# Kernel optimization log

Measured on AMD Instinct MI355X. Metric: run time of the kernel, lower is better.

Reference implementation:

```python
import jax, jax.numpy as jnp
import numpy as np

N_USER, N_ITEM, D = 50000, 30000, 64
N = N_USER + N_ITEM
NNZ_UI, NNZ_R, NNZ_II = 1000000, 800000, 300000
IMG_F, TXT_F = 512, 384
EPS = 1e-5


def spmm(rows, cols, vals, x, n_out):
    # sparse [n_out, n_in] @ dense [n_in, d] via gather + segment-sum
    return jax.ops.segment_sum(vals[:, None] * x[cols], rows, num_segments=n_out)


def leaky_relu(x):
    return jnp.where(x >= 0, x, 0.01 * x)


def setup_inputs() -> dict:
    key = jax.random.key(0)
    ks = jax.random.split(key, 32)
    f = lambda i, shape, s=0.05: (jax.random.normal(ks[i], shape, dtype=jnp.float32) * s)
    inp = {
        'user_emb': f(0, (N_USER, D)),
        'item_emb': f(1, (N_ITEM, D)),
        'image_embedding': f(2, (N_ITEM, IMG_F), 1.0),
        'text_embedding': f(3, (N_ITEM, TXT_F), 1.0),
        'W_img': f(4, (IMG_F, D)), 'b_img': jnp.zeros((D,), jnp.float32),
        'bn_g_img': jnp.ones((D,), jnp.float32), 'bn_b_img': jnp.zeros((D,), jnp.float32),
        'W_txt': f(5, (TXT_F, D)), 'b_txt': jnp.zeros((D,), jnp.float32),
        'bn_g_txt': jnp.ones((D,), jnp.float32), 'bn_b_txt': jnp.zeros((D,), jnp.float32),
        'W_gate_img': f(6, (D, D)), 'b_gate_img': jnp.zeros((D,), jnp.float32),
        'W_gate_txt': f(7, (D, D)), 'b_gate_txt': jnp.zeros((D,), jnp.float32),
        'W_common1': f(8, (D, D)), 'b_common1': jnp.zeros((D,), jnp.float32),
        'w_common2': f(9, (D,)),
        'ui_vals': jax.random.uniform(ks[10], (NNZ_UI,), dtype=jnp.float32),
        'R_vals': jax.random.uniform(ks[11], (NNZ_R,), dtype=jnp.float32),
        'ii_img_vals': jax.random.uniform(ks[12], (NNZ_II,), dtype=jnp.float32),
        'ii_txt_vals': jax.random.uniform(ks[13], (NNZ_II,), dtype=jnp.float32),
        'ui_rows': jax.random.randint(ks[14], (NNZ_UI,), 0, N, dtype=jnp.int32),
        'ui_cols': jax.random.randint(ks[15], (NNZ_UI,), 0, N, dtype=jnp.int32),
        'R_rows': jax.random.randint(ks[16], (NNZ_R,), 0, N_USER, dtype=jnp.int32),
        'R_cols': jax.random.randint(ks[17], (NNZ_R,), 0, N_ITEM, dtype=jnp.int32),
        'ii_img_rows': jax.random.randint(ks[18], (NNZ_II,), 0, N_ITEM, dtype=jnp.int32),
        'ii_img_cols': jax.random.randint(ks[19], (NNZ_II,), 0, N_ITEM, dtype=jnp.int32),
        'ii_txt_rows': jax.random.randint(ks[20], (NNZ_II,), 0, N_ITEM, dtype=jnp.int32),
        'ii_txt_cols': jax.random.randint(ks[21], (NNZ_II,), 0, N_ITEM, dtype=jnp.int32),
    }
    return inp


def reference(user_emb, item_emb, image_embedding, text_embedding,
              W_img, b_img, bn_g_img, bn_b_img,
              W_txt, b_txt, bn_g_txt, bn_b_txt,
              W_gate_img, b_gate_img, W_gate_txt, b_gate_txt,
              W_common1, b_common1, w_common2,
              ui_vals, R_vals, ii_img_vals, ii_txt_vals,
              ui_rows, ui_cols, R_rows, R_cols,
              ii_img_rows, ii_img_cols, ii_txt_rows, ii_txt_cols):
    # ---- user_item_GCN: adj = original + diffusion (fused edge list) ----
    cat = jnp.concatenate([item_emb, user_emb], axis=0)  # [N, D], item first per source
    embs = [cat]
    for _ in range(2):
        cat = spmm(ui_rows, ui_cols, ui_vals, cat, N)
        embs.append(cat)
    content_embedding = jnp.stack(embs, axis=1).mean(axis=1)  # [N, D]

    # ---- modal projections (BN inference, dropout=eval identity) ----
    def project(x, W, b, g, beta):
        h = x @ W + b
        h = h * (g / jnp.sqrt(1.0 + EPS)) + beta  # BatchNorm1d, running stats (0, 1)
        return leaky_relu(h)

    img_feat = project(image_embedding, W_img, b_img, bn_g_img, bn_b_img)  # [I, D]
    txt_feat = project(text_embedding, W_txt, b_txt, bn_g_txt, bn_b_txt)

    # ---- item_item_GCN ----
    def modal_branch(feat, Wg, bg, rows, cols, vals):
        it = item_emb * jax.nn.sigmoid(feat @ Wg + bg)  # gated item embedding
        for _ in range(2):
            it = spmm(rows, cols, vals, it, N_ITEM)
        us = spmm(R_rows, R_cols, R_vals, it, N_USER)  # R @ item -> user
        return jnp.concatenate([us, it], axis=0)  # [N, D], user first per source

    image_ui = modal_branch(img_feat, W_gate_img, b_gate_img, ii_img_rows, ii_img_cols, ii_img_vals)
    text_ui = modal_branch(txt_feat, W_gate_txt, b_gate_txt, ii_txt_rows, ii_txt_cols, ii_txt_vals)

    # ---- gate_attention_fusion (non-tiktok: 2 modalities) ----
    def att_score(e):
        return leaky_relu(e @ W_common1 + b_common1) @ w_common2  # [N]

    att = jnp.stack([att_score(image_ui), att_score(text_ui)], axis=-1)  # [N, 2]
    w = jax.nn.softmax(att, axis=-1)
    common = w[:, 0:1] * image_ui + w[:, 1:2] * text_ui
    special_img = image_ui - common
    special_txt = text_ui - common

    return jnp.stack([content_embedding, special_img, special_txt, common], axis=0)  # [4, N, D]
```

## Files before the change

kernel.cpp:

```cpp
#include <hip/hip_runtime.h>

#define N_USER 50000
#define N_ITEM 30000
#define DIM    64
#define NTOT   80000
#define NNZ_UI 1000000
#define NNZ_R  800000
#define NNZ_II 300000
#define IMG_F  512
#define TXT_F  384

#define NROWS_ALL 190000
#define NNZ_ALL   2400000
#define BASE_R    NTOT
#define BASE_II   (NTOT + N_USER)
#define BASE_IT   (NTOT + N_USER + N_ITEM)

#define RB_BITS   9
#define RB_ROWS   512
#define NBUCK     ((NROWS_ALL + RB_ROWS - 1) / RB_ROWS)
#define NBLK_A2   400
#define EDG_A2    6000

#define NBLK_PG   625
#define NBLK_UIP  5000
#define NBLK_I16  1875
#define NBLK_U16  3125

__device__ __forceinline__ int edge_row(int i,
        const int* __restrict__ r0, const int* __restrict__ r1,
        const int* __restrict__ r2, const int* __restrict__ r3){
    if (i < NNZ_UI)                       return r0[i];
    if (i < NNZ_UI + NNZ_R)               return BASE_R  + r1[i - NNZ_UI];
    if (i < NNZ_UI + NNZ_R + NNZ_II)      return BASE_II + r2[i - NNZ_UI - NNZ_R];
    return BASE_IT + r3[i - NNZ_UI - NNZ_R - NNZ_II];
}

__device__ __forceinline__ void edge_all(int i,
        const int* __restrict__ r0, const int* __restrict__ c0, const float* __restrict__ v0,
        const int* __restrict__ r1, const int* __restrict__ c1, const float* __restrict__ v1,
        const int* __restrict__ r2, const int* __restrict__ c2, const float* __restrict__ v2,
        const int* __restrict__ r3, const int* __restrict__ c3, const float* __restrict__ v3,
        int& gr, int& col, float& val){
    if (i < NNZ_UI){
        gr = r0[i]; col = c0[i]; val = v0[i];
    } else if (i < NNZ_UI + NNZ_R){
        int j = i - NNZ_UI;               gr = BASE_R  + r1[j]; col = c1[j]; val = v1[j];
    } else if (i < NNZ_UI + NNZ_R + NNZ_II){
        int j = i - NNZ_UI - NNZ_R;       gr = BASE_II + r2[j]; col = c2[j]; val = v2[j];
    } else {
        int j = i - NNZ_UI - NNZ_R - NNZ_II; gr = BASE_IT + r3[j]; col = c3[j]; val = v3[j];
    }
}

__global__ __launch_bounds__(256) void k_bhist(const int* __restrict__ r0,
        const int* __restrict__ r1, const int* __restrict__ r2,
        const int* __restrict__ r3, int* __restrict__ bcnt){
    __shared__ int h[NBUCK];
    for (int i = threadIdx.x; i < NBUCK; i += 256) h[i] = 0;
    __syncthreads();
    const int stride = gridDim.x * 256;
    for (int i = blockIdx.x * 256 + threadIdx.x; i < NNZ_ALL; i += stride){
        int gr = edge_row(i, r0, r1, r2, r3);
        atomicAdd(&h[gr >> RB_BITS], 1);
    }
    __syncthreads();
    for (int i = threadIdx.x; i < NBUCK; i += 256){
        int c = h[i];
        if (c) atomicAdd(&bcnt[i], c);
    }
}

__global__ __launch_bounds__(512) void k_bscan(const int* __restrict__ bcnt,
        int* __restrict__ bbase, int* __restrict__ off){
    __shared__ int sh[512];
    const int t = threadIdx.x;
    int v = (t < NBUCK) ? bcnt[t] : 0;
    sh[t] = v;
    __syncthreads();
    for (int d = 1; d < 512; d <<= 1){
        int u = (t >= d) ? sh[t - d] : 0;
        __syncthreads();
        sh[t] += u;
        __syncthreads();
    }
    if (t < NBUCK) bbase[t] = sh[t] - v;
    if (t == NBUCK - 1){
        bbase[NBUCK] = sh[t];
        off[NROWS_ALL] = sh[t];
    }
}

__global__ __launch_bounds__(256) void k_bin(
        const int* __restrict__ r0, const int* __restrict__ c0, const float* __restrict__ v0,
        const int* __restrict__ r1, const int* __restrict__ c1, const float* __restrict__ v1,
        const int* __restrict__ r2, const int* __restrict__ c2, const float* __restrict__ v2,
        const int* __restrict__ r3, const int* __restrict__ c3, const float* __restrict__ v3,
        const int* __restrict__ bbase, int* __restrict__ bcur,
        int2* __restrict__ binned){
    __shared__ int lofs[NBUCK];
    __shared__ int lcur[NBUCK];
    const int t = threadIdx.x;
    for (int i = t; i < NBUCK; i += 256){ lofs[i] = 0; lcur[i] = 0; }
    __syncthreads();
    const int s0 = blockIdx.x * EDG_A2, s1 = s0 + EDG_A2;
    for (int i = s0 + t; i < s1; i += 256){
        int gr = edge_row(i, r0, r1, r2, r3);
        atomicAdd(&lofs[gr >> RB_BITS], 1);
    }
    __syncthreads();
    for (int i = t; i < NBUCK; i += 256){
        int c = lofs[i];
        lofs[i] = c ? (bbase[i] + atomicAdd(&bcur[i], c)) : 0;
    }
    __syncthreads();
    for (int i = s0 + t; i < s1; i += 256){
        int gr, col; float val;
        edge_all(i, r0, c0, v0, r1, c1, v1, r2, c2, v2, r3, c3, v3, gr, col, val);
        int b = gr >> RB_BITS;
        int slot = atomicAdd(&lcur[b], 1);
        binned[lofs[b] + slot] = make_int2((col << RB_BITS) | (gr & (RB_ROWS - 1)),
                                           __float_as_int(val));
    }
}

__global__ __launch_bounds__(256) void k_scatter(const int* __restrict__ bbase,
        const int2* __restrict__ binned, int* __restrict__ off,
        int2* __restrict__ csr){
    __shared__ int h[RB_ROWS];
    const int t = threadIdx.x;
    const int b = blockIdx.x;
    const int base = bbase[b];
    const int nb = bbase[b + 1] - base;
    h[t] = 0; h[t + 256] = 0;
    __syncthreads();
    for (int i = t; i < nb; i += 256)
        atomicAdd(&h[binned[base + i].x & (RB_ROWS - 1)], 1);
    __syncthreads();
    if (t < 64){
        int v[8], s = 0;
#pragma unroll
        for (int k = 0; k < 8; ++k){ v[k] = h[t * 8 + k]; s += v[k]; }
        int incl = s;
#pragma unroll
        for (int d = 1; d < 64; d <<= 1){
            int u = __shfl_up(incl, d, 64);
            if (t >= d) incl += u;
        }
        int run = incl - s;
#pragma unroll
        for (int k = 0; k < 8; ++k){ int tmp = v[k]; h[t * 8 + k] = run; run += tmp; }
    }
    __syncthreads();
    const int row0 = b << RB_BITS;
    for (int i = t; i < RB_ROWS; i += 256){
        int r = row0 + i;
        if (r < NROWS_ALL) off[r] = base + h[i];
    }
    __syncthreads();
    for (int i = t; i < nb; i += 256){
        int2 rec = binned[base + i];
        int lr = rec.x & (RB_ROWS - 1);
        int slot = atomicAdd(&h[lr], 1);
        csr[base + slot] = make_int2(rec.x >> RB_BITS, rec.y);
    }
}

__device__ __forceinline__ const float* cat_row(int c,
        const float* __restrict__ item, const float* __restrict__ user){
    return (c < N_ITEM) ? (item + ((long)c << 6)) : (user + ((long)(c - N_ITEM) << 6));
}

__device__ __forceinline__ void pull_body(const int* __restrict__ off,
        const int2* __restrict__ csr, const float* __restrict__ x,
        float* __restrict__ y, int r, int l){
    int s = off[r], e = off[r + 1];
    float4 a0 = {0.f, 0.f, 0.f, 0.f};
    float4 a1 = {0.f, 0.f, 0.f, 0.f};
    int j = s;
    for (; j + 2 <= e; j += 2){
        int2 e0 = csr[j];
        int2 e1 = csr[j + 1];
        float v0 = __int_as_float(e0.y);
        float v1 = __int_as_float(e1.y);
        const float4 x0 = *reinterpret_cast<const float4*>(x + ((long)e0.x << 6) + l);
        const float4 x1 = *reinterpret_cast<const float4*>(x + ((long)e1.x << 6) + l);
        a0.x = fmaf(v0, x0.x, a0.x);
        a0.y = fmaf(v0, x0.y, a0.y);
        a0.z = fmaf(v0, x0.z, a0.z);
        a0.w = fmaf(v0, x0.w, a0.w);
        a1.x = fmaf(v1, x1.x, a1.x);
        a1.y = fmaf(v1, x1.y, a1.y);
        a1.z = fmaf(v1, x1.z, a1.z);
        a1.w = fmaf(v1, x1.w, a1.w);
    }
    if (j < e){
        int2 e0 = csr[j];
        float v0 = __int_as_float(e0.y);
        const float4 x0 = *reinterpret_cast<const float4*>(x + ((long)e0.x << 6) + l);
        a0.x = fmaf(v0, x0.x, a0.x);
        a0.y = fmaf(v0, x0.y, a0.y);
        a0.z = fmaf(v0, x0.z, a0.z);
        a0.w = fmaf(v0, x0.w, a0.w);
    }
    a0.x += a1.x; a0.y += a1.y; a0.z += a1.z; a0.w += a1.w;
    *reinterpret_cast<float4*>(y + ((long)r << 6) + l) = a0;
}

__device__ __forceinline__ void pull_cat_body(const int* __restrict__ off,
        const int2* __restrict__ csr, const float* __restrict__ item,
        const float* __restrict__ user, float* __restrict__ y, int r, int l){
    int s = off[r], e = off[r + 1];
    float4 a0 = {0.f, 0.f, 0.f, 0.f};
    float4 a1 = {0.f, 0.f, 0.f, 0.f};
    int j = s;
    for (; j + 2 <= e; j += 2){
        int2 e0 = csr[j];
        int2 e1 = csr[j + 1];
        float v0 = __int_as_float(e0.y);
        float v1 = __int_as_float(e1.y);
        const float4 x0 = *reinterpret_cast<const float4*>(cat_row(e0.x, item, user) + l);
        const float4 x1 = *reinterpret_cast<const float4*>(cat_row(e1.x, item, user) + l);
        a0.x = fmaf(v0, x0.x, a0.x);
        a0.y = fmaf(v0, x0.y, a0.y);
        a0.z = fmaf(v0, x0.z, a0.z);
        a0.w = fmaf(v0, x0.w, a0.w);
        a1.x = fmaf(v1, x1.x, a1.x);
        a1.y = fmaf(v1, x1.y, a1.y);
        a1.z = fmaf(v1, x1.z, a1.z);
        a1.w = fmaf(v1, x1.w, a1.w);
    }
    if (j < e){
        int2 e0 = csr[j];
        float v0 = __int_as_float(e0.y);
        const float4 x0 = *reinterpret_cast<const float4*>(cat_row(e0.x, item, user) + l);
        a0.x = fmaf(v0, x0.x, a0.x);
        a0.y = fmaf(v0, x0.y, a0.y);
        a0.z = fmaf(v0, x0.z, a0.z);
        a0.w = fmaf(v0, x0.w, a0.w);
    }
    a0.x += a1.x; a0.y += a1.y; a0.z += a1.z; a0.w += a1.w;
    *reinterpret_cast<float4*>(y + ((long)r << 6) + l) = a0;
}

__global__ void k_pull2(const int* __restrict__ offA, const int2* __restrict__ csr,
                        const float* __restrict__ xA, float* __restrict__ yA,
                        const int* __restrict__ offB, const float* __restrict__ xB,
                        float* __restrict__ yB, int nrows, int nblk_half){
    int b = blockIdx.x;
    const int* off; const float* x; float* y;
    if (b < nblk_half){ off = offA; x = xA; y = yA; }
    else              { b -= nblk_half; off = offB; x = xB; y = yB; }
    int t = b * 256 + threadIdx.x;
    int r = t >> 4;
    if (r >= nrows) return;
    pull_body(off, csr, x, y, r, (t & 15) << 2);
}

__global__ void k_pullR(const int* __restrict__ off, const int2* __restrict__ csr,
                        const float* __restrict__ xA, float* __restrict__ yA,
                        const float* __restrict__ xB, float* __restrict__ yB,
                        int nrows){
    int t = blockIdx.x * 256 + threadIdx.x;
    int r = t >> 4;
    if (r >= nrows) return;
    int l = (t & 15) << 2;
    int s = off[r], e = off[r + 1];
    float4 pA0 = {0.f,0.f,0.f,0.f}, pA1 = {0.f,0.f,0.f,0.f};
    float4 pB0 = {0.f,0.f,0.f,0.f}, pB1 = {0.f,0.f,0.f,0.f};
    int j = s;
    for (; j + 2 <= e; j += 2){
        int2 e0 = csr[j];
        int2 e1 = csr[j + 1];
        float v0 = __int_as_float(e0.y);
        float v1 = __int_as_float(e1.y);
        long o0 = ((long)e0.x << 6) + l;
        long o1 = ((long)e1.x << 6) + l;
        const float4 xa0 = *reinterpret_cast<const float4*>(xA + o0);
        const float4 xa1 = *reinterpret_cast<const float4*>(xA + o1);
        const float4 xb0 = *reinterpret_cast<const float4*>(xB + o0);
        const float4 xb1 = *reinterpret_cast<const float4*>(xB + o1);
        pA0.x = fmaf(v0, xa0.x, pA0.x); pA0.y = fmaf(v0, xa0.y, pA0.y);
        pA0.z = fmaf(v0, xa0.z, pA0.z); pA0.w = fmaf(v0, xa0.w, pA0.w);
        pA1.x = fmaf(v1, xa1.x, pA1.x); pA1.y = fmaf(v1, xa1.y, pA1.y);
        pA1.z = fmaf(v1, xa1.z, pA1.z); pA1.w = fmaf(v1, xa1.w, pA1.w);
        pB0.x = fmaf(v0, xb0.x, pB0.x); pB0.y = fmaf(v0, xb0.y, pB0.y);
        pB0.z = fmaf(v0, xb0.z, pB0.z); pB0.w = fmaf(v0, xb0.w, pB0.w);
        pB1.x = fmaf(v1, xb1.x, pB1.x); pB1.y = fmaf(v1, xb1.y, pB1.y);
        pB1.z = fmaf(v1, xb1.z, pB1.z); pB1.w = fmaf(v1, xb1.w, pB1.w);
    }
    if (j < e){
        int2 e0 = csr[j];
        float v0 = __int_as_float(e0.y);
        long o0 = ((long)e0.x << 6) + l;
        const float4 xa0 = *reinterpret_cast<const float4*>(xA + o0);
        const float4 xb0 = *reinterpret_cast<const float4*>(xB + o0);
        pA0.x = fmaf(v0, xa0.x, pA0.x); pA0.y = fmaf(v0, xa0.y, pA0.y);
        pA0.z = fmaf(v0, xa0.z, pA0.z); pA0.w = fmaf(v0, xa0.w, pA0.w);
        pB0.x = fmaf(v0, xb0.x, pB0.x); pB0.y = fmaf(v0, xb0.y, pB0.y);
        pB0.z = fmaf(v0, xb0.z, pB0.z); pB0.w = fmaf(v0, xb0.w, pB0.w);
    }
    pA0.x += pA1.x; pA0.y += pA1.y; pA0.z += pA1.z; pA0.w += pA1.w;
    pB0.x += pB1.x; pB0.y += pB1.y; pB0.z += pB1.z; pB0.w += pB1.w;
    *reinterpret_cast<float4*>(yA + ((long)r << 6) + l) = pA0;
    *reinterpret_cast<float4*>(yB + ((long)r << 6) + l) = pB0;
}

__global__ void k_pull_mean_cat(const int* __restrict__ off, const int2* __restrict__ csr,
        const float* __restrict__ x, const float* __restrict__ item,
        const float* __restrict__ user, float* __restrict__ o0, int nrows){
    int t = blockIdx.x * 256 + threadIdx.x;
    int r = t >> 4;
    if (r >= nrows) return;
    int l = (t & 15) << 2;
    int s = off[r], e = off[r + 1];
    float4 a0 = {0.f, 0.f, 0.f, 0.f};
    float4 a1 = {0.f, 0.f, 0.f, 0.f};
    int j = s;
    for (; j + 2 <= e; j += 2){
        int2 e0 = csr[j];
        int2 e1 = csr[j + 1];
        float v0 = __int_as_float(e0.y);
        float v1 = __int_as_float(e1.y);
        const float4 x0 = *reinterpret_cast<const float4*>(x + ((long)e0.x << 6) + l);
        const float4 x1 = *reinterpret_cast<const float4*>(x + ((long)e1.x << 6) + l);
        a0.x = fmaf(v0, x0.x, a0.x);
        a0.y = fmaf(v0, x0.y, a0.y);
        a0.z = fmaf(v0, x0.z, a0.z);
        a0.w = fmaf(v0, x0.w, a0.w);
        a1.x = fmaf(v1, x1.x, a1.x);
        a1.y = fmaf(v1, x1.y, a1.y);
        a1.z = fmaf(v1, x1.z, a1.z);
        a1.w = fmaf(v1, x1.w, a1.w);
    }
    if (j < e){
        int2 e0 = csr[j];
        float v0 = __int_as_float(e0.y);
        const float4 x0 = *reinterpret_cast<const float4*>(x + ((long)e0.x << 6) + l);
        a0.x = fmaf(v0, x0.x, a0.x);
        a0.y = fmaf(v0, x0.y, a0.y);
        a0.z = fmaf(v0, x0.z, a0.z);
        a0.w = fmaf(v0, x0.w, a0.w);
    }
    const float4 av = *reinterpret_cast<const float4*>(cat_row(r, item, user) + l);
    const float4 xv = *reinterpret_cast<const float4*>(x + ((long)r << 6) + l);
    float4 o;
    o.x = (av.x + xv.x + a0.x + a1.x) * (1.0f / 3.0f);
    o.y = (av.y + xv.y + a0.y + a1.y) * (1.0f / 3.0f);
    o.z = (av.z + xv.z + a0.z + a1.z) * (1.0f / 3.0f);
    o.w = (av.w + xv.w + a0.w + a1.w) * (1.0f / 3.0f);
    *reinterpret_cast<float4*>(o0 + ((long)r << 6) + l) = o;
}

__global__ __launch_bounds__(256) void k_mega1(
        const int* __restrict__ offUI, const int2* __restrict__ csr,
        const float* __restrict__ user,
        float* __restrict__ hop1out,
        const float* __restrict__ Xi, const float* __restrict__ Wi,
        const float* __restrict__ bi, const float* __restrict__ gi,
        const float* __restrict__ bei, const float* __restrict__ Wgi,
        const float* __restrict__ bgi,
        const float* __restrict__ Xt, const float* __restrict__ Wt,
        const float* __restrict__ bt, const float* __restrict__ gt,
        const float* __restrict__ bet, const float* __restrict__ Wgt,
        const float* __restrict__ bgt,
        const float* __restrict__ item,
        float* __restrict__ Pi, float* __restrict__ Pt){
    __shared__ float xs[48][68];
    __shared__ float ws[64][64];

    if (blockIdx.x < NBLK_UIP){
        int t = blockIdx.x * 256 + threadIdx.x;
        int r = t >> 4;
        pull_cat_body(offUI, csr, item, user, hop1out, r, (t & 15) << 2);
        return;
    }

    const int t  = threadIdx.x;
    const int tr = t >> 4;
    const int tc = t & 15;
    const int pgb = blockIdx.x - NBLK_UIP;
    const bool isTxt = pgb >= NBLK_PG;
    const int  blk   = isTxt ? (pgb - NBLK_PG) : pgb;
    const int  K     = isTxt ? TXT_F : IMG_F;
    const float* X   = isTxt ? Xt  : Xi;
    const float* W   = isTxt ? Wt  : Wi;
    const float* bb  = isTxt ? bt  : bi;
    const float* gg  = isTxt ? gt  : gi;
    const float* be  = isTxt ? bet : bei;
    const float* Wg  = isTxt ? Wgt : Wgi;
    const float* bg  = isTxt ? bgt : bgi;
    float* outP      = isTxt ? Pt  : Pi;
    const int row0   = blk * 48;

    float acc[3][4];
#pragma unroll
    for (int i = 0; i < 3; ++i)
#pragma unroll
        for (int j = 0; j < 4; ++j) acc[i][j] = 0.f;

    for (int ks = 0; ks < K; ks += 64){
        __syncthreads();
#pragma unroll
        for (int i = 0; i < 3; ++i){
            int r = tr + 16 * i;
            *reinterpret_cast<float4*>(&xs[r][tc * 4]) =
                *reinterpret_cast<const float4*>(X + (long)(row0 + r) * K + ks + tc * 4);
        }
        {
            const float4* wsrc = reinterpret_cast<const float4*>(W + (long)ks * 64);
            float4* wdst = reinterpret_cast<float4*>(&ws[0][0]);
#pragma unroll
            for (int i = 0; i < 4; ++i) wdst[t + 256 * i] = wsrc[t + 256 * i];
        }
        __syncthreads();
#pragma unroll 8
        for (int kk = 0; kk < 64; kk += 2){
            float2 a[3];
#pragma unroll
            for (int i = 0; i < 3; ++i)
                a[i] = *reinterpret_cast<const float2*>(&xs[tr + 16 * i][kk]);
            float4 b0 = *reinterpret_cast<const float4*>(&ws[kk][tc * 4]);
            float4 b1 = *reinterpret_cast<const float4*>(&ws[kk + 1][tc * 4]);
#pragma unroll
            for (int i = 0; i < 3; ++i){
                acc[i][0] = fmaf(a[i].x, b0.x, acc[i][0]);
                acc[i][1] = fmaf(a[i].x, b0.y, acc[i][1]);
                acc[i][2] = fmaf(a[i].x, b0.z, acc[i][2]);
                acc[i][3] = fmaf(a[i].x, b0.w, acc[i][3]);
                acc[i][0] = fmaf(a[i].y, b1.x, acc[i][0]);
                acc[i][1] = fmaf(a[i].y, b1.y, acc[i][1]);
                acc[i][2] = fmaf(a[i].y, b1.z, acc[i][2]);
                acc[i][3] = fmaf(a[i].y, b1.w, acc[i][3]);
            }
        }
    }

    const float4 b4  = reinterpret_cast<const float4*>(bb)[tc];
    const float4 g4  = reinterpret_cast<const float4*>(gg)[tc];
    const float4 be4 = reinterpret_cast<const float4*>(be)[tc];
    __syncthreads();
#pragma unroll
    for (int i = 0; i < 3; ++i){
        int r = tr + 16 * i;
        float4 h;
        h.x = (acc[i][0] + b4.x) * (g4.x * 0.99999500003749943f) + be4.x;
        h.y = (acc[i][1] + b4.y) * (g4.y * 0.99999500003749943f) + be4.y;
        h.z = (acc[i][2] + b4.z) * (g4.z * 0.99999500003749943f) + be4.z;
        h.w = (acc[i][3] + b4.w) * (g4.w * 0.99999500003749943f) + be4.w;
        h.x = (h.x >= 0.f) ? h.x : 0.01f * h.x;
        h.y = (h.y >= 0.f) ? h.y : 0.01f * h.y;
        h.z = (h.z >= 0.f) ? h.z : 0.01f * h.z;
        h.w = (h.w >= 0.f) ? h.w : 0.01f * h.w;
        *reinterpret_cast<float4*>(&xs[r][tc * 4]) = h;
    }
    {
        const float4* wsrc = reinterpret_cast<const float4*>(Wg);
        float4* wdst = reinterpret_cast<float4*>(&ws[0][0]);
#pragma unroll
        for (int i = 0; i < 4; ++i) wdst[t + 256 * i] = wsrc[t + 256 * i];
    }
    __syncthreads();

    float ac2[3][4];
#pragma unroll
    for (int i = 0; i < 3; ++i)
#pragma unroll
        for (int j = 0; j < 4; ++j) ac2[i][j] = 0.f;
#pragma unroll 8
    for (int kk = 0; kk < 64; kk += 2){
        float2 a[3];
#pragma unroll
        for (int i = 0; i < 3; ++i)
            a[i] = *reinterpret_cast<const float2*>(&xs[tr + 16 * i][kk]);
        float4 b0 = *reinterpret_cast<const float4*>(&ws[kk][tc * 4]);
        float4 b1 = *reinterpret_cast<const float4*>(&ws[kk + 1][tc * 4]);
#pragma unroll
        for (int i = 0; i < 3; ++i){
            ac2[i][0] = fmaf(a[i].x, b0.x, ac2[i][0]);
            ac2[i][1] = fmaf(a[i].x, b0.y, ac2[i][1]);
            ac2[i][2] = fmaf(a[i].x, b0.z, ac2[i][2]);
            ac2[i][3] = fmaf(a[i].x, b0.w, ac2[i][3]);
            ac2[i][0] = fmaf(a[i].y, b1.x, ac2[i][0]);
            ac2[i][1] = fmaf(a[i].y, b1.y, ac2[i][1]);
            ac2[i][2] = fmaf(a[i].y, b1.z, ac2[i][2]);
            ac2[i][3] = fmaf(a[i].y, b1.w, ac2[i][3]);
        }
    }

    const float4 bg4 = reinterpret_cast<const float4*>(bg)[tc];
#pragma unroll
    for (int i = 0; i < 3; ++i){
        int r = tr + 16 * i;
        const float4 iv = *reinterpret_cast<const float4*>(
                item + (long)(row0 + r) * 64 + tc * 4);
        float4 o;
        o.x = iv.x / (1.f + __expf(-(ac2[i][0] + bg4.x)));
        o.y = iv.y / (1.f + __expf(-(ac2[i][1] + bg4.y)));
        o.z = iv.z / (1.f + __expf(-(ac2[i][2] + bg4.z)));
        o.w = iv.w / (1.f + __expf(-(ac2[i][3] + bg4.w)));
        *reinterpret_cast<float4*>(outP + (long)(row0 + r) * 64 + tc * 4) = o;
    }
}

__global__ __launch_bounds__(256) void k_fuse(const float* __restrict__ img,
        const float* __restrict__ txt, const float* __restrict__ W1,
        const float* __restrict__ b1, const float* __restrict__ w2,
        float* __restrict__ out){
    __shared__ float si[64][68];
    __shared__ float st[64][68];
    __shared__ float w1s[64][64];
    const int t  = threadIdx.x;
    const int tr = t >> 4;
    const int tc = t & 15;
    const long row0 = (long)blockIdx.x * 64;

#pragma unroll
    for (int i = 0; i < 4; ++i){
        int r = tr + 16 * i;
        *reinterpret_cast<float4*>(&si[r][tc * 4]) =
            *reinterpret_cast<const float4*>(img + (row0 + r) * 64 + tc * 4);
        *reinterpret_cast<float4*>(&st[r][tc * 4]) =
            *reinterpret_cast<const float4*>(txt + (row0 + r) * 64 + tc * 4);
    }
    {
        const float4* wsrc = reinterpret_cast<const float4*>(W1);
        float4* wdst = reinterpret_cast<float4*>(&w1s[0][0]);
#pragma unroll
        for (int i = 0; i < 4; ++i) wdst[t + 256 * i] = wsrc[t + 256 * i];
    }
    __syncthreads();

    float ai[4][4], at[4][4];
#pragma unroll
    for (int i = 0; i < 4; ++i)
#pragma unroll
        for (int j = 0; j < 4; ++j){ ai[i][j] = 0.f; at[i][j] = 0.f; }

#pragma unroll 8
    for (int kk = 0; kk < 64; kk += 2){
        float4 b0 = *reinterpret_cast<const float4*>(&w1s[kk][tc * 4]);
        float4 b1v = *reinterpret_cast<const float4*>(&w1s[kk + 1][tc * 4]);
#pragma unroll
        for (int i = 0; i < 4; ++i){
            float2 a = *reinterpret_cast<const float2*>(&si[tr + 16 * i][kk]);
            float2 c = *reinterpret_cast<const float2*>(&st[tr + 16 * i][kk]);
            ai[i][0] = fmaf(a.x, b0.x, ai[i][0]);
            ai[i][1] = fmaf(a.x, b0.y, ai[i][1]);
            ai[i][2] = fmaf(a.x, b0.z, ai[i][2]);
            ai[i][3] = fmaf(a.x, b0.w, ai[i][3]);
            ai[i][0] = fmaf(a.y, b1v.x, ai[i][0]);
            ai[i][1] = fmaf(a.y, b1v.y, ai[i][1]);
            ai[i][2] = fmaf(a.y, b1v.z, ai[i][2]);
            ai[i][3] = fmaf(a.y, b1v.w, ai[i][3]);
            at[i][0] = fmaf(c.x, b0.x, at[i][0]);
            at[i][1] = fmaf(c.x, b0.y, at[i][1]);
            at[i][2] = fmaf(c.x, b0.z, at[i][2]);
            at[i][3] = fmaf(c.x, b0.w, at[i][3]);
            at[i][0] = fmaf(c.y, b1v.x, at[i][0]);
            at[i][1] = fmaf(c.y, b1v.y, at[i][1]);
            at[i][2] = fmaf(c.y, b1v.z, at[i][2]);
            at[i][3] = fmaf(c.y, b1v.w, at[i][3]);
        }
    }

    const float4 b14 = reinterpret_cast<const float4*>(b1)[tc];
    const float4 w24 = reinterpret_cast<const float4*>(w2)[tc];
    float pi[4], pt[4];
#pragma unroll
    for (int i = 0; i < 4; ++i){
        float hi0 = ai[i][0] + b14.x; hi0 = (hi0 >= 0.f) ? hi0 : 0.01f * hi0;
        float hi1 = ai[i][1] + b14.y; hi1 = (hi1 >= 0.f) ? hi1 : 0.01f * hi1;
        float hi2 = ai[i][2] + b14.z; hi2 = (hi2 >= 0.f) ? hi2 : 0.01f * hi2;
        float hi3 = ai[i][3] + b14.w; hi3 = (hi3 >= 0.f) ? hi3 : 0.01f * hi3;
        float ht0 = at[i][0] + b14.x; ht0 = (ht0 >= 0.f) ? ht0 : 0.01f * ht0;
        float ht1 = at[i][1] + b14.y; ht1 = (ht1 >= 0.f) ? ht1 : 0.01f * ht1;
        float ht2 = at[i][2] + b14.z; ht2 = (ht2 >= 0.f) ? ht2 : 0.01f * ht2;
        float ht3 = at[i][3] + b14.w; ht3 = (ht3 >= 0.f) ? ht3 : 0.01f * ht3;
        pi[i] = fmaf(hi0, w24.x, fmaf(hi1, w24.y, fmaf(hi2, w24.z, hi3 * w24.w)));
        pt[i] = fmaf(ht0, w24.x, fmaf(ht1, w24.y, fmaf(ht2, w24.z, ht3 * w24.w)));
    }
#pragma unroll
    for (int m = 1; m < 16; m <<= 1){
#pragma unroll
        for (int i = 0; i < 4; ++i){
            pi[i] += __shfl_xor(pi[i], m, 64);
            pt[i] += __shfl_xor(pt[i], m, 64);
        }
    }

    const long NTD = (long)NTOT * DIM;
#pragma unroll
    for (int i = 0; i < 4; ++i){
        int r = tr + 16 * i;
        float mx = fmaxf(pi[i], pt[i]);
        float ei = __expf(pi[i] - mx), et = __expf(pt[i] - mx);
        float inv = 1.f / (ei + et);
        float wi = ei * inv, wt = et * inv;
        const float4 ie = *reinterpret_cast<const float4*>(&si[r][tc * 4]);
        const float4 te = *reinterpret_cast<const float4*>(&st[r][tc * 4]);
        float4 cm, oi, ot;
        cm.x = wi * ie.x + wt * te.x;
        cm.y = wi * ie.y + wt * te.y;
        cm.z = wi * ie.z + wt * te.z;
        cm.w = wi * ie.w + wt * te.w;
        oi.x = ie.x - cm.x; oi.y = ie.y - cm.y; oi.z = ie.z - cm.z; oi.w = ie.w - cm.w;
        ot.x = te.x - cm.x; ot.y = te.y - cm.y; ot.z = te.z - cm.z; ot.w = te.w - cm.w;
        long o = (row0 + r) * 64 + tc * 4;
        *reinterpret_cast<float4*>(out + NTD + o)     = oi;
        *reinterpret_cast<float4*>(out + 2 * NTD + o) = ot;
        *reinterpret_cast<float4*>(out + 3 * NTD + o) = cm;
    }
}

extern "C" void kernel_launch(void* const* d_in, const int* in_sizes, int n_in,
                              void* d_out, int out_size, void* d_ws, size_t ws_size,
                              hipStream_t stream){
    const float* user_emb  = (const float*)d_in[0];
    const float* item_emb  = (const float*)d_in[1];
    const float* image_emb = (const float*)d_in[2];
    const float* text_emb  = (const float*)d_in[3];
    const float* W_img = (const float*)d_in[4];
    const float* b_img = (const float*)d_in[5];
    const float* g_img = (const float*)d_in[6];
    const float* be_img= (const float*)d_in[7];
    const float* W_txt = (const float*)d_in[8];
    const float* b_txt = (const float*)d_in[9];
    const float* g_txt = (const float*)d_in[10];
    const float* be_txt= (const float*)d_in[11];
    const float* W_gi  = (const float*)d_in[12];
    const float* b_gi  = (const float*)d_in[13];
    const float* W_gt  = (const float*)d_in[14];
    const float* b_gt  = (const float*)d_in[15];
    const float* W_c1  = (const float*)d_in[16];
    const float* b_c1  = (const float*)d_in[17];
    const float* w_c2  = (const float*)d_in[18];
    const float* ui_vals = (const float*)d_in[19];
    const float* R_vals  = (const float*)d_in[20];
    const float* ii_iv   = (const float*)d_in[21];
    const float* ii_tv   = (const float*)d_in[22];
    const int* ui_rows = (const int*)d_in[23];
    const int* ui_cols = (const int*)d_in[24];
    const int* R_rows  = (const int*)d_in[25];
    const int* R_cols  = (const int*)d_in[26];
    const int* ii_ir   = (const int*)d_in[27];
    const int* ii_ic   = (const int*)d_in[28];
    const int* ii_tr   = (const int*)d_in[29];
    const int* ii_tc   = (const int*)d_in[30];

    const long ND = (long)NTOT * DIM;
    const long ID = (long)N_ITEM * DIM;
    const long UD = (long)N_USER * DIM;

    float* out = (float*)d_out;
    float* o0 = out;
    float* o1 = out + ND;
    float* o2 = out + 2 * ND;
    float* o3 = out + 3 * ND;

    float* P_img = o3;
    float* P_txt = o3 + ID;
    float* Q_img = o2;
    float* Q_txt = o1;

    int2* binned = (int2*)o0;

    int2* csr   = (int2*)d_ws;
    int*  off   = (int*)(csr + NNZ_ALL);
    int*  bcnt  = off + NROWS_ALL + 4;
    int*  bcur  = bcnt + NBUCK;
    int*  bbase = bcur + NBUCK;

    hipMemsetAsync(bcnt, 0, 2 * NBUCK * sizeof(int), stream);
    k_bhist<<<512, 256, 0, stream>>>(ui_rows, R_rows, ii_ir, ii_tr, bcnt);
    k_bscan<<<1, 512, 0, stream>>>(bcnt, bbase, off);
    k_bin<<<NBLK_A2, 256, 0, stream>>>(
        ui_rows, ui_cols, ui_vals,  R_rows, R_cols, R_vals,
        ii_ir, ii_ic, ii_iv,        ii_tr, ii_tc, ii_tv,
        bbase, bcur, binned);
    k_scatter<<<NBUCK, 256, 0, stream>>>(bbase, binned, off, csr);

    const int* offUI = off;
    const int* offR  = off + BASE_R;
    const int* offI2 = off + BASE_II;
    const int* offT2 = off + BASE_IT;

    k_mega1<<<NBLK_UIP + 2 * NBLK_PG, 256, 0, stream>>>(
        offUI, csr, user_emb, o2,
        image_emb, W_img, b_img, g_img, be_img, W_gi, b_gi,
        text_emb,  W_txt, b_txt, g_txt, be_txt, W_gt, b_gt,
        item_emb, P_img, P_txt);

    k_pull_mean_cat<<<NBLK_UIP, 256, 0, stream>>>(
        offUI, csr, o2, item_emb, user_emb, o0, NTOT);

    k_pull2<<<2 * NBLK_I16, 256, 0, stream>>>(
        offI2, csr, P_img, Q_img, offT2, P_txt, Q_txt, N_ITEM, NBLK_I16);
    k_pull2<<<2 * NBLK_I16, 256, 0, stream>>>(
        offI2, csr, Q_img, o1 + UD, offT2, Q_txt, o2 + UD, N_ITEM, NBLK_I16);
    k_pullR<<<NBLK_U16, 256, 0, stream>>>(
        offR, csr, o1 + UD, o1, o2 + UD, o2, N_USER);

    k_fuse<<<NTOT / 64, 256, 0, stream>>>(o1, o2, W_c1, b_c1, w_c2, out);
}
```

Baseline: 562.9 us.

## Fuse first item-item hop with mean pull and interleave block types

The mean/concat pull over the UI graph now runs in one kernel with the first item-item SpMM hop for both modalities, with blocks interleaved 4:3. Block ordering in the first mega kernel is interleaved 4:1 between pull blocks and projection blocks so the two work types overlap. Intermediate buffers are remapped so the second hop writes to scratch in o3. The final R-pull kernel also copies the item rows into the outputs, which drops one launch but adds an explicit copy of the item embeddings.

```diff
diff --git a/kernel.cpp b/kernel.cpp
--- a/kernel.cpp
+++ b/kernel.cpp
@@ -26,6 +26,11 @@
 #define NBLK_UIP  5000
 #define NBLK_I16  1875
 #define NBLK_U16  3125
+#define NBLK_CP   1875
+
+#define NBLK_M1   (NBLK_UIP + 2 * NBLK_PG)
+#define NBLK_M2   (NBLK_UIP + 2 * NBLK_I16)
+#define NBLK_RC   (NBLK_U16 + 2 * NBLK_CP)
 
 __device__ __forceinline__ int edge_row(int i,
         const int* __restrict__ r0, const int* __restrict__ r1,
@@ -243,6 +248,49 @@
     *reinterpret_cast<float4*>(y + ((long)r << 6) + l) = a0;
 }
 
+__device__ __forceinline__ void pull_mean_body(const int* __restrict__ off,
+        const int2* __restrict__ csr, const float* __restrict__ x,
+        const float* __restrict__ item, const float* __restrict__ user,
+        float* __restrict__ o0, int r, int l){
+    int s = off[r], e = off[r + 1];
+    float4 a0 = {0.f, 0.f, 0.f, 0.f};
+    float4 a1 = {0.f, 0.f, 0.f, 0.f};
+    int j = s;
+    for (; j + 2 <= e; j += 2){
+        int2 e0 = csr[j];
+        int2 e1 = csr[j + 1];
+        float v0 = __int_as_float(e0.y);
+        float v1 = __int_as_float(e1.y);
+        const float4 x0 = *reinterpret_cast<const float4*>(x + ((long)e0.x << 6) + l);
+        const float4 x1 = *reinterpret_cast<const float4*>(x + ((long)e1.x << 6) + l);
+        a0.x = fmaf(v0, x0.x, a0.x);
+        a0.y = fmaf(v0, x0.y, a0.y);
+        a0.z = fmaf(v0, x0.z, a0.z);
+        a0.w = fmaf(v0, x0.w, a0.w);
+        a1.x = fmaf(v1, x1.x, a1.x);
+        a1.y = fmaf(v1, x1.y, a1.y);
+        a1.z = fmaf(v1, x1.z, a1.z);
+        a1.w = fmaf(v1, x1.w, a1.w);
+    }
+    if (j < e){
+        int2 e0 = csr[j];
+        float v0 = __int_as_float(e0.y);
+        const float4 x0 = *reinterpret_cast<const float4*>(x + ((long)e0.x << 6) + l);
+        a0.x = fmaf(v0, x0.x, a0.x);
+        a0.y = fmaf(v0, x0.y, a0.y);
+        a0.z = fmaf(v0, x0.z, a0.z);
+        a0.w = fmaf(v0, x0.w, a0.w);
+    }
+    const float4 av = *reinterpret_cast<const float4*>(cat_row(r, item, user) + l);
+    const float4 xv = *reinterpret_cast<const float4*>(x + ((long)r << 6) + l);
+    float4 o;
+    o.x = (av.x + xv.x + a0.x + a1.x) * (1.0f / 3.0f);
+    o.y = (av.y + xv.y + a0.y + a1.y) * (1.0f / 3.0f);
+    o.z = (av.z + xv.z + a0.z + a1.z) * (1.0f / 3.0f);
+    o.w = (av.w + xv.w + a0.w + a1.w) * (1.0f / 3.0f);
+    *reinterpret_cast<float4*>(o0 + ((long)r << 6) + l) = o;
+}
+
 __global__ void k_pull2(const int* __restrict__ offA, const int2* __restrict__ csr,
                         const float* __restrict__ xA, float* __restrict__ yA,
                         const int* __restrict__ offB, const float* __restrict__ xB,
@@ -257,13 +305,207 @@
     pull_body(off, csr, x, y, r, (t & 15) << 2);
 }
 
-__global__ void k_pullR(const int* __restrict__ off, const int2* __restrict__ csr,
-                        const float* __restrict__ xA, float* __restrict__ yA,
-                        const float* __restrict__ xB, float* __restrict__ yB,
-                        int nrows){
-    int t = blockIdx.x * 256 + threadIdx.x;
+__global__ __launch_bounds__(256) void k_mega1(
+        const int* __restrict__ offUI, const int2* __restrict__ csr,
+        const float* __restrict__ user,
+        float* __restrict__ hop1out,
+        const float* __restrict__ Xi, const float* __restrict__ Wi,
+        const float* __restrict__ bi, const float* __restrict__ gi,
+        const float* __restrict__ bei, const float* __restrict__ Wgi,
+        const float* __restrict__ bgi,
+        const float* __restrict__ Xt, const float* __restrict__ Wt,
+        const float* __restrict__ bt, const float* __restrict__ gt,
+        const float* __restrict__ bet, const float* __restrict__ Wgt,
+        const float* __restrict__ bgt,
+        const float* __restrict__ item,
+        float* __restrict__ Pi, float* __restrict__ Pt){
+    __shared__ float xs[48][68];
+    __shared__ float ws[64][64];
+
+    const int r5 = blockIdx.x % 5;
+    const int q5 = blockIdx.x / 5;
+
+    if (r5 < 4){
+        int pb = q5 * 4 + r5;
+        int t = pb * 256 + threadIdx.x;
+        int r = t >> 4;
+        pull_cat_body(offUI, csr, item, user, hop1out, r, (t & 15) << 2);
+        return;
+    }
+
+    const int t  = threadIdx.x;
+    const int tr = t >> 4;
+    const int tc = t & 15;
+    const int pgb = q5;
+    const bool isTxt = pgb >= NBLK_PG;
+    const int  blk   = isTxt ? (pgb - NBLK_PG) : pgb;
+    const int  K     = isTxt ? TXT_F : IMG_F;
+    const float* X   = isTxt ? Xt  : Xi;
+    const float* W   = isTxt ? Wt  : Wi;
+    const float* bb  = isTxt ? bt  : bi;
+    const float* gg  = isTxt ? gt  : gi;
+    const float* be  = isTxt ? bet : bei;
+    const float* Wg  = isTxt ? Wgt : Wgi;
+    const float* bg  = isTxt ? bgt : bgi;
+    float* outP      = isTxt ? Pt  : Pi;
+    const int row0   = blk * 48;
+
+    float acc[3][4];
+#pragma unroll
+    for (int i = 0; i < 3; ++i)
+#pragma unroll
+        for (int j = 0; j < 4; ++j) acc[i][j] = 0.f;
+
+    for (int ks = 0; ks < K; ks += 64){
+        __syncthreads();
+#pragma unroll
+        for (int i = 0; i < 3; ++i){
+            int r = tr + 16 * i;
+            *reinterpret_cast<float4*>(&xs[r][tc * 4]) =
+                *reinterpret_cast<const float4*>(X + (long)(row0 + r) * K + ks + tc * 4);
+        }
+        {
+            const float4* wsrc = reinterpret_cast<const float4*>(W + (long)ks * 64);
+            float4* wdst = reinterpret_cast<float4*>(&ws[0][0]);
+#pragma unroll
+            for (int i = 0; i < 4; ++i) wdst[t + 256 * i] = wsrc[t + 256 * i];
+        }
+        __syncthreads();
+#pragma unroll 8
+        for (int kk = 0; kk < 64; kk += 2){
+            float2 a[3];
+#pragma unroll
+            for (int i = 0; i < 3; ++i)
+                a[i] = *reinterpret_cast<const float2*>(&xs[tr + 16 * i][kk]);
+            float4 b0 = *reinterpret_cast<const float4*>(&ws[kk][tc * 4]);
+            float4 b1 = *reinterpret_cast<const float4*>(&ws[kk + 1][tc * 4]);
+#pragma unroll
+            for (int i = 0; i < 3; ++i){
+                acc[i][0] = fmaf(a[i].x, b0.x, acc[i][0]);
+                acc[i][1] = fmaf(a[i].x, b0.y, acc[i][1]);
+                acc[i][2] = fmaf(a[i].x, b0.z, acc[i][2]);
+                acc[i][3] = fmaf(a[i].x, b0.w, acc[i][3]);
+                acc[i][0] = fmaf(a[i].y, b1.x, acc[i][0]);
+                acc[i][1] = fmaf(a[i].y, b1.y, acc[i][1]);
+                acc[i][2] = fmaf(a[i].y, b1.z, acc[i][2]);
+                acc[i][3] = fmaf(a[i].y, b1.w, acc[i][3]);
+            }
+        }
+    }
+
+    const float4 b4  = reinterpret_cast<const float4*>(bb)[tc];
+    const float4 g4  = reinterpret_cast<const float4*>(gg)[tc];
+    const float4 be4 = reinterpret_cast<const float4*>(be)[tc];
+    __syncthreads();
+#pragma unroll
+    for (int i = 0; i < 3; ++i){
+        int r = tr + 16 * i;
+        float4 h;
+        h.x = (acc[i][0] + b4.x) * (g4.x * 0.99999500003749943f) + be4.x;
+        h.y = (acc[i][1] + b4.y) * (g4.y * 0.99999500003749943f) + be4.y;
+        h.z = (acc[i][2] + b4.z) * (g4.z * 0.99999500003749943f) + be4.z;
+        h.w = (acc[i][3] + b4.w) * (g4.w * 0.99999500003749943f) + be4.w;
+        h.x = (h.x >= 0.f) ? h.x : 0.01f * h.x;
+        h.y = (h.y >= 0.f) ? h.y : 0.01f * h.y;
+        h.z = (h.z >= 0.f) ? h.z : 0.01f * h.z;
+        h.w = (h.w >= 0.f) ? h.w : 0.01f * h.w;
+        *reinterpret_cast<float4*>(&xs[r][tc * 4]) = h;
+    }
+    {
+        const float4* wsrc = reinterpret_cast<const float4*>(Wg);
+        float4* wdst = reinterpret_cast<float4*>(&ws[0][0]);
+#pragma unroll
+        for (int i = 0; i < 4; ++i) wdst[t + 256 * i] = wsrc[t + 256 * i];
+    }
+    __syncthreads();
+
+    float ac2[3][4];
+#pragma unroll
+    for (int i = 0; i < 3; ++i)
+#pragma unroll
+        for (int j = 0; j < 4; ++j) ac2[i][j] = 0.f;
+#pragma unroll 8
+    for (int kk = 0; kk < 64; kk += 2){
+        float2 a[3];
+#pragma unroll
+        for (int i = 0; i < 3; ++i)
+            a[i] = *reinterpret_cast<const float2*>(&xs[tr + 16 * i][kk]);
+        float4 b0 = *reinterpret_cast<const float4*>(&ws[kk][tc * 4]);
+        float4 b1 = *reinterpret_cast<const float4*>(&ws[kk + 1][tc * 4]);
+#pragma unroll
+        for (int i = 0; i < 3; ++i){
+            ac2[i][0] = fmaf(a[i].x, b0.x, ac2[i][0]);
+            ac2[i][1] = fmaf(a[i].x, b0.y, ac2[i][1]);
+            ac2[i][2] = fmaf(a[i].x, b0.z, ac2[i][2]);
+            ac2[i][3] = fmaf(a[i].x, b0.w, ac2[i][3]);
+            ac2[i][0] = fmaf(a[i].y, b1.x, ac2[i][0]);
+            ac2[i][1] = fmaf(a[i].y, b1.y, ac2[i][1]);
+            ac2[i][2] = fmaf(a[i].y, b1.z, ac2[i][2]);
+            ac2[i][3] = fmaf(a[i].y, b1.w, ac2[i][3]);
+        }
+    }
+
+    const float4 bg4 = reinterpret_cast<const float4*>(bg)[tc];
+#pragma unroll
+    for (int i = 0; i < 3; ++i){
+        int r = tr + 16 * i;
+        const float4 iv = *reinterpret_cast<const float4*>(
+                item + (long)(row0 + r) * 64 + tc * 4);
+        float4 o;
+        o.x = iv.x / (1.f + __expf(-(ac2[i][0] + bg4.x)));
+        o.y = iv.y / (1.f + __expf(-(ac2[i][1] + bg4.y)));
+        o.z = iv.z / (1.f + __expf(-(ac2[i][2] + bg4.z)));
+        o.w = iv.w / (1.f + __expf(-(ac2[i][3] + bg4.w)));
+        *reinterpret_cast<float4*>(outP + (long)(row0 + r) * 64 + tc * 4) = o;
+    }
+}
+
+__global__ void k_mega2(const int* __restrict__ offUI, const int2* __restrict__ csr,
+        const float* __restrict__ hop1,
+        const float* __restrict__ item, const float* __restrict__ user,
+        float* __restrict__ o0,
+        const int* __restrict__ offI2, const float* __restrict__ P_img,
+        float* __restrict__ Q_img,
+        const int* __restrict__ offT2, const float* __restrict__ P_txt,
+        float* __restrict__ Q_txt){
+    const int r7 = blockIdx.x % 7;
+    const int q7 = blockIdx.x / 7;
+    const int tid = threadIdx.x;
+    if (r7 < 4){
+        int pb = q7 * 4 + r7;
+        int t = pb * 256 + tid;
+        int r = t >> 4;
+        pull_mean_body(offUI, csr, hop1, item, user, o0, r, (t & 15) << 2);
+    } else {
+        int m = q7 * 3 + (r7 - 4);
+        const int* off; const float* x; float* y;
+        if (m < NBLK_I16){ off = offI2; x = P_img; y = Q_img; }
+        else             { m -= NBLK_I16; off = offT2; x = P_txt; y = Q_txt; }
+        int t = m * 256 + tid;
+        int r = t >> 4;
+        pull_body(off, csr, x, y, r, (t & 15) << 2);
+    }
+}
+
+__global__ void k_pullRC(const int* __restrict__ off, const int2* __restrict__ csr,
+                         const float* __restrict__ xA, float* __restrict__ yA,
+                         const float* __restrict__ xB, float* __restrict__ yB,
+                         float* __restrict__ dA, float* __restrict__ dB){
+    int bid = blockIdx.x;
+    const int tid = threadIdx.x;
+    if (bid >= NBLK_U16){
+        int c = bid - NBLK_U16;
+        const float4* src; float4* dst;
+        if (c < NBLK_CP){ src = reinterpret_cast<const float4*>(xA);
+                          dst = reinterpret_cast<float4*>(dA); }
+        else { c -= NBLK_CP; src = reinterpret_cast<const float4*>(xB);
+               dst = reinterpret_cast<float4*>(dB); }
+        int i = c * 256 + tid;
+        dst[i] = src[i];
+        return;
+    }
+    int t = bid * 256 + tid;
     int r = t >> 4;
-    if (r >= nrows) return;
     int l = (t & 15) << 2;
     int s = off[r], e = off[r + 1];
     float4 pA0 = {0.f,0.f,0.f,0.f}, pA1 = {0.f,0.f,0.f,0.f};
@@ -304,203 +546,6 @@
     pB0.x += pB1.x; pB0.y += pB1.y; pB0.z += pB1.z; pB0.w += pB1.w;
     *reinterpret_cast<float4*>(yA + ((long)r << 6) + l) = pA0;
     *reinterpret_cast<float4*>(yB + ((long)r << 6) + l) = pB0;
-}
-
-__global__ void k_pull_mean_cat(const int* __restrict__ off, const int2* __restrict__ csr,
-        const float* __restrict__ x, const float* __restrict__ item,
-        const float* __restrict__ user, float* __restrict__ o0, int nrows){
-    int t = blockIdx.x * 256 + threadIdx.x;
-    int r = t >> 4;
-    if (r >= nrows) return;
-    int l = (t & 15) << 2;
-    int s = off[r], e = off[r + 1];
-    float4 a0 = {0.f, 0.f, 0.f, 0.f};
-    float4 a1 = {0.f, 0.f, 0.f, 0.f};
-    int j = s;
-    for (; j + 2 <= e; j += 2){
-        int2 e0 = csr[j];
-        int2 e1 = csr[j + 1];
-        float v0 = __int_as_float(e0.y);
-        float v1 = __int_as_float(e1.y);
-        const float4 x0 = *reinterpret_cast<const float4*>(x + ((long)e0.x << 6) + l);
-        const float4 x1 = *reinterpret_cast<const float4*>(x + ((long)e1.x << 6) + l);
-        a0.x = fmaf(v0, x0.x, a0.x);
-        a0.y = fmaf(v0, x0.y, a0.y);
-        a0.z = fmaf(v0, x0.z, a0.z);
-        a0.w = fmaf(v0, x0.w, a0.w);
-        a1.x = fmaf(v1, x1.x, a1.x);
-        a1.y = fmaf(v1, x1.y, a1.y);
-        a1.z = fmaf(v1, x1.z, a1.z);
-        a1.w = fmaf(v1, x1.w, a1.w);
-    }
-    if (j < e){
-        int2 e0 = csr[j];
-        float v0 = __int_as_float(e0.y);
-        const float4 x0 = *reinterpret_cast<const float4*>(x + ((long)e0.x << 6) + l);
-        a0.x = fmaf(v0, x0.x, a0.x);
-        a0.y = fmaf(v0, x0.y, a0.y);
-        a0.z = fmaf(v0, x0.z, a0.z);
-        a0.w = fmaf(v0, x0.w, a0.w);
-    }
-    const float4 av = *reinterpret_cast<const float4*>(cat_row(r, item, user) + l);
-    const float4 xv = *reinterpret_cast<const float4*>(x + ((long)r << 6) + l);
-    float4 o;
-    o.x = (av.x + xv.x + a0.x + a1.x) * (1.0f / 3.0f);
-    o.y = (av.y + xv.y + a0.y + a1.y) * (1.0f / 3.0f);
-    o.z = (av.z + xv.z + a0.z + a1.z) * (1.0f / 3.0f);
-    o.w = (av.w + xv.w + a0.w + a1.w) * (1.0f / 3.0f);
-    *reinterpret_cast<float4*>(o0 + ((long)r << 6) + l) = o;
-}
-
-__global__ __launch_bounds__(256) void k_mega1(
-        const int* __restrict__ offUI, const int2* __restrict__ csr,
-        const float* __restrict__ user,
-        float* __restrict__ hop1out,
-        const float* __restrict__ Xi, const float* __restrict__ Wi,
-        const float* __restrict__ bi, const float* __restrict__ gi,
-        const float* __restrict__ bei, const float* __restrict__ Wgi,
-        const float* __restrict__ bgi,
-        const float* __restrict__ Xt, const float* __restrict__ Wt,
-        const float* __restrict__ bt, const float* __restrict__ gt,
-        const float* __restrict__ bet, const float* __restrict__ Wgt,
-        const float* __restrict__ bgt,
-        const float* __restrict__ item,
-        float* __restrict__ Pi, float* __restrict__ Pt){
-    __shared__ float xs[48][68];
-    __shared__ float ws[64][64];
-
-    if (blockIdx.x < NBLK_UIP){
-        int t = blockIdx.x * 256 + threadIdx.x;
-        int r = t >> 4;
-        pull_cat_body(offUI, csr, item, user, hop1out, r, (t & 15) << 2);
-        return;
-    }
-
-    const int t  = threadIdx.x;
-    const int tr = t >> 4;
-    const int tc = t & 15;
-    const int pgb = blockIdx.x - NBLK_UIP;
-    const bool isTxt = pgb >= NBLK_PG;
-    const int  blk   = isTxt ? (pgb - NBLK_PG) : pgb;
-    const int  K     = isTxt ? TXT_F : IMG_F;
-    const float* X   = isTxt ? Xt  : Xi;
-    const float* W   = isTxt ? Wt  : Wi;
-    const float* bb  = isTxt ? bt  : bi;
-    const float* gg  = isTxt ? gt  : gi;
-    const float* be  = isTxt ? bet : bei;
-    const float* Wg  = isTxt ? Wgt : Wgi;
-    const float* bg  = isTxt ? bgt : bgi;
-    float* outP      = isTxt ? Pt  : Pi;
-    const int row0   = blk * 48;
-
-    float acc[3][4];
-#pragma unroll
-    for (int i = 0; i < 3; ++i)
-#pragma unroll
-        for (int j = 0; j < 4; ++j) acc[i][j] = 0.f;
-
-    for (int ks = 0; ks < K; ks += 64){
-        __syncthreads();
-#pragma unroll
-        for (int i = 0; i < 3; ++i){
-            int r = tr + 16 * i;
-            *reinterpret_cast<float4*>(&xs[r][tc * 4]) =
-                *reinterpret_cast<const float4*>(X + (long)(row0 + r) * K + ks + tc * 4);
-        }
-        {
-            const float4* wsrc = reinterpret_cast<const float4*>(W + (long)ks * 64);
-            float4* wdst = reinterpret_cast<float4*>(&ws[0][0]);
-#pragma unroll
-            for (int i = 0; i < 4; ++i) wdst[t + 256 * i] = wsrc[t + 256 * i];
-        }
-        __syncthreads();
-#pragma unroll 8
-        for (int kk = 0; kk < 64; kk += 2){
-            float2 a[3];
-#pragma unroll
-            for (int i = 0; i < 3; ++i)
-                a[i] = *reinterpret_cast<const float2*>(&xs[tr + 16 * i][kk]);
-            float4 b0 = *reinterpret_cast<const float4*>(&ws[kk][tc * 4]);
-            float4 b1 = *reinterpret_cast<const float4*>(&ws[kk + 1][tc * 4]);
-#pragma unroll
-            for (int i = 0; i < 3; ++i){
-                acc[i][0] = fmaf(a[i].x, b0.x, acc[i][0]);
-                acc[i][1] = fmaf(a[i].x, b0.y, acc[i][1]);
-                acc[i][2] = fmaf(a[i].x, b0.z, acc[i][2]);
-                acc[i][3] = fmaf(a[i].x, b0.w, acc[i][3]);
-                acc[i][0] = fmaf(a[i].y, b1.x, acc[i][0]);
-                acc[i][1] = fmaf(a[i].y, b1.y, acc[i][1]);
-                acc[i][2] = fmaf(a[i].y, b1.z, acc[i][2]);
-                acc[i][3] = fmaf(a[i].y, b1.w, acc[i][3]);
-            }
-        }
-    }
-
-    const float4 b4  = reinterpret_cast<const float4*>(bb)[tc];
-    const float4 g4  = reinterpret_cast<const float4*>(gg)[tc];
-    const float4 be4 = reinterpret_cast<const float4*>(be)[tc];
-    __syncthreads();
-#pragma unroll
-    for (int i = 0; i < 3; ++i){
-        int r = tr + 16 * i;
-        float4 h;
-        h.x = (acc[i][0] + b4.x) * (g4.x * 0.99999500003749943f) + be4.x;
-        h.y = (acc[i][1] + b4.y) * (g4.y * 0.99999500003749943f) + be4.y;
-        h.z = (acc[i][2] + b4.z) * (g4.z * 0.99999500003749943f) + be4.z;
-        h.w = (acc[i][3] + b4.w) * (g4.w * 0.99999500003749943f) + be4.w;
-        h.x = (h.x >= 0.f) ? h.x : 0.01f * h.x;
-        h.y = (h.y >= 0.f) ? h.y : 0.01f * h.y;
-        h.z = (h.z >= 0.f) ? h.z : 0.01f * h.z;
-        h.w = (h.w >= 0.f) ? h.w : 0.01f * h.w;
-        *reinterpret_cast<float4*>(&xs[r][tc * 4]) = h;
-    }
-    {
-        const float4* wsrc = reinterpret_cast<const float4*>(Wg);
-        float4* wdst = reinterpret_cast<float4*>(&ws[0][0]);
-#pragma unroll
-        for (int i = 0; i < 4; ++i) wdst[t + 256 * i] = wsrc[t + 256 * i];
-    }
-    __syncthreads();
-
-    float ac2[3][4];
-#pragma unroll
-    for (int i = 0; i < 3; ++i)
-#pragma unroll
-        for (int j = 0; j < 4; ++j) ac2[i][j] = 0.f;
-#pragma unroll 8
-    for (int kk = 0; kk < 64; kk += 2){
-        float2 a[3];
-#pragma unroll
-        for (int i = 0; i < 3; ++i)
-            a[i] = *reinterpret_cast<const float2*>(&xs[tr + 16 * i][kk]);
-        float4 b0 = *reinterpret_cast<const float4*>(&ws[kk][tc * 4]);
-        float4 b1 = *reinterpret_cast<const float4*>(&ws[kk + 1][tc * 4]);
-#pragma unroll
-        for (int i = 0; i < 3; ++i){
-            ac2[i][0] = fmaf(a[i].x, b0.x, ac2[i][0]);
-            ac2[i][1] = fmaf(a[i].x, b0.y, ac2[i][1]);
-            ac2[i][2] = fmaf(a[i].x, b0.z, ac2[i][2]);
-            ac2[i][3] = fmaf(a[i].x, b0.w, ac2[i][3]);
-            ac2[i][0] = fmaf(a[i].y, b1.x, ac2[i][0]);
-            ac2[i][1] = fmaf(a[i].y, b1.y, ac2[i][1]);
-            ac2[i][2] = fmaf(a[i].y, b1.z, ac2[i][2]);
-            ac2[i][3] = fmaf(a[i].y, b1.w, ac2[i][3]);
-        }
-    }
-
-    const float4 bg4 = reinterpret_cast<const float4*>(bg)[tc];
-#pragma unroll
-    for (int i = 0; i < 3; ++i){
-        int r = tr + 16 * i;
-        const float4 iv = *reinterpret_cast<const float4*>(
-                item + (long)(row0 + r) * 64 + tc * 4);
-        float4 o;
-        o.x = iv.x / (1.f + __expf(-(ac2[i][0] + bg4.x)));
-        o.y = iv.y / (1.f + __expf(-(ac2[i][1] + bg4.y)));
-        o.z = iv.z / (1.f + __expf(-(ac2[i][2] + bg4.z)));
-        o.w = iv.w / (1.f + __expf(-(ac2[i][3] + bg4.w)));
-        *reinterpret_cast<float4*>(outP + (long)(row0 + r) * 64 + tc * 4) = o;
-    }
 }
 
 __global__ __launch_bounds__(256) void k_fuse(const float* __restrict__ img,
@@ -660,8 +705,10 @@
 
     float* P_img = o3;
     float* P_txt = o3 + ID;
-    float* Q_img = o2;
-    float* Q_txt = o1;
+    float* Q_img = o1;
+    float* Q_txt = o1 + ID;
+    float* H_img = o3;
+    float* H_txt = o3 + ID;
 
     int2* binned = (int2*)o0;
 
@@ -685,21 +732,21 @@
     const int* offI2 = off + BASE_II;
     const int* offT2 = off + BASE_IT;
 
-    k_mega1<<<NBLK_UIP + 2 * NBLK_PG, 256, 0, stream>>>(
+    k_mega1<<<NBLK_M1, 256, 0, stream>>>(
         offUI, csr, user_emb, o2,
         image_emb, W_img, b_img, g_img, be_img, W_gi, b_gi,
         text_emb,  W_txt, b_txt, g_txt, be_txt, W_gt, b_gt,
         item_emb, P_img, P_txt);
 
-    k_pull_mean_cat<<<NBLK_UIP, 256, 0, stream>>>(
-        offUI, csr, o2, item_emb, user_emb, o0, NTOT);
+    k_mega2<<<NBLK_M2, 256, 0, stream>>>(
+        offUI, csr, o2, item_emb, user_emb, o0,
+        offI2, P_img, Q_img, offT2, P_txt, Q_txt);
 
     k_pull2<<<2 * NBLK_I16, 256, 0, stream>>>(
-        offI2, csr, P_img, Q_img, offT2, P_txt, Q_txt, N_ITEM, NBLK_I16);
-    k_pull2<<<2 * NBLK_I16, 256, 0, stream>>>(
-        offI2, csr, Q_img, o1 + UD, offT2, Q_txt, o2 + UD, N_ITEM, NBLK_I16);
-    k_pullR<<<NBLK_U16, 256, 0, stream>>>(
-        offR, csr, o1 + UD, o1, o2 + UD, o2, N_USER);
+        offI2, csr, Q_img, H_img, offT2, Q_txt, H_txt, N_ITEM, NBLK_I16);
+
+    k_pullRC<<<NBLK_RC, 256, 0, stream>>>(
+        offR, csr, H_img, o1, H_txt, o2, o1 + UD, o2 + UD);
 
     k_fuse<<<NTOT / 64, 256, 0, stream>>>(o1, o2, W_c1, b_c1, w_c2, out);
 }
```

Result: slower. 575.2 us (+2.2%).
